# Optimization experiments

Measured on AMD Instinct MI355X. Metric: run time of the kernel, lower is better.

The kernel has to match this reference:

```python
import jax, jax.numpy as jnp
import numpy as np

EPS = 1e-12

def setup_inputs() -> dict:
    key = jax.random.key(0)
    k1, k2, k3 = jax.random.split(key, 3)
    B, D, N, NCLS = 1024, 512, 100000, 1000
    z = jax.random.normal(k1, (B, D), dtype=jnp.float32)
    lab_bank = jax.random.normal(k2, (N, D), dtype=jnp.float32)
    lab_labels = jax.random.randint(k3, (N,), 0, NCLS, dtype=jnp.int64)
    return {"z": z, "lab_bank": lab_bank, "lab_labels": lab_labels, "topk": 5}

def reference(z, lab_bank, lab_labels, topk):
    # cosine similarity: normalize query and bank, then GEMM
    zn = z / jnp.maximum(jnp.linalg.norm(z, axis=-1, keepdims=True), EPS)            # [B, D]
    bn = lab_bank / jnp.maximum(jnp.linalg.norm(lab_bank, axis=-1, keepdims=True), EPS)  # [N, D]
    sim = jnp.einsum('bd,nd->bn', zn, bn)                                            # [B, N]
    top_vals, top_idx = jax.lax.top_k(sim, topk)                                     # [B, k] each
    labels = lab_labels[top_idx]                                                     # [B, k]
    return top_idx, top_vals, labels
```

## Files before the change

kernel.cpp:

```cpp
#include <hip/hip_runtime.h>
#include <math.h>

#define DDIM 512
#define NS 96
#define SPITCH 132
#define KMASK 0xFFFFF800
#define NEG_INF (-3.0e38f)
#define IMAX 0x7fffffff

typedef __fp16   h16x2 __attribute__((ext_vector_type(2)));
typedef _Float16 f16x8 __attribute__((ext_vector_type(8)));
typedef float    f32x4 __attribute__((ext_vector_type(4)));
typedef int      i32x4 __attribute__((ext_vector_type(4)));

__device__ __forceinline__ int imin(int a, int b) { return a < b ? a : b; }
__device__ __forceinline__ int imax(int a, int b) { return a > b ? a : b; }

__device__ __forceinline__ void glds16(const void* g, void* l) {
    __builtin_amdgcn_global_load_lds((const __attribute__((address_space(1))) void*)g,
                                     (__attribute__((address_space(3))) void*)l, 16, 0, 0);
}

__global__ __launch_bounds__(256) void split_tile_k(const float* __restrict__ src,
                                                    unsigned* __restrict__ tile,
                                                    float* __restrict__ rn, int rows) {
    const int t = threadIdx.x;
    const int r = t >> 1, hf = t & 1;
    const int R = blockIdx.x * 128 + r;
    const bool valid = R < rows;
    const float* srow = src + (size_t)(valid ? R : 0) * DDIM + hf * 16;
    float ss = 0.f;
    for (int ks = 0; ks < 16; ++ks) {
        float4 v0 = *(const float4*)(srow + ks * 32);
        float4 v1 = *(const float4*)(srow + ks * 32 + 4);
        float4 v2 = *(const float4*)(srow + ks * 32 + 8);
        float4 v3 = *(const float4*)(srow + ks * 32 + 12);
        ss += v0.x*v0.x + v0.y*v0.y + v0.z*v0.z + v0.w*v0.w
            + v1.x*v1.x + v1.y*v1.y + v1.z*v1.z + v1.w*v1.w
            + v2.x*v2.x + v2.y*v2.y + v2.z*v2.z + v2.w*v2.w
            + v3.x*v3.x + v3.y*v3.y + v3.z*v3.z + v3.w*v3.w;
        unsigned o[8];
        o[0] = __builtin_bit_cast(unsigned, __builtin_amdgcn_cvt_pkrtz(v0.x, v0.y));
        o[1] = __builtin_bit_cast(unsigned, __builtin_amdgcn_cvt_pkrtz(v0.z, v0.w));
        o[2] = __builtin_bit_cast(unsigned, __builtin_amdgcn_cvt_pkrtz(v1.x, v1.y));
        o[3] = __builtin_bit_cast(unsigned, __builtin_amdgcn_cvt_pkrtz(v1.z, v1.w));
        o[4] = __builtin_bit_cast(unsigned, __builtin_amdgcn_cvt_pkrtz(v2.x, v2.y));
        o[5] = __builtin_bit_cast(unsigned, __builtin_amdgcn_cvt_pkrtz(v2.z, v2.w));
        o[6] = __builtin_bit_cast(unsigned, __builtin_amdgcn_cvt_pkrtz(v3.x, v3.y));
        o[7] = __builtin_bit_cast(unsigned, __builtin_amdgcn_cvt_pkrtz(v3.z, v3.w));
        if (!valid) {
            #pragma unroll
            for (int q = 0; q < 8; ++q) o[q] = 0u;
        }
        unsigned* dst = tile + ((size_t)(blockIdx.x * 16 + ks) * 128 + r) * 16 + hf * 8;
        *(i32x4*)dst       = *(i32x4*)o;
        *(i32x4*)(dst + 4) = *(i32x4*)(o + 4);
    }
    ss += __shfl_xor(ss, 1, 64);
    if (valid && hf == 0) rn[R] = 1.0f / fmaxf(sqrtf(ss), 1e-12f);
}

__global__ __launch_bounds__(256, 3) void gemm_screen_k(
    const unsigned* __restrict__ zh, const unsigned* __restrict__ bh,
    const float* __restrict__ rb,
    int* __restrict__ cand, int N, int nChunks) {

    __shared__ alignas(16) int smem[8448];
    int* SIMI = smem;

    const int t = threadIdx.x;
    const int w = t >> 6, lane = t & 63;
    const int wm = w & 1, wn = w >> 1;
    const int quad = lane >> 4, l16 = lane & 15;
    const int split = blockIdx.x, rowblk = blockIdx.y;
    const int soff = w * 1024 + lane * 16;

    int t0 = (int)0x80000000, t1 = t0, t2 = t0, t3 = t0;

    int iter = 0;
    for (int chunk = split; chunk < nChunks; chunk += NS, ++iter) {
        f32x4 acc[4][4];
        #pragma unroll
        for (int mi = 0; mi < 4; ++mi)
            #pragma unroll
            for (int ni = 0; ni < 4; ++ni) acc[mi][ni] = (f32x4){0.f, 0.f, 0.f, 0.f};

        for (int ks = 0; ks < 16; ++ks) {
            __syncthreads();
            const char* gA = (const char*)zh + ((size_t)(rowblk * 16 + ks) * 8192);
            const char* gB = (const char*)bh + ((size_t)(chunk * 16 + ks) * 8192);
            glds16(gA + soff,        (char*)smem + soff);
            glds16(gA + 4096 + soff, (char*)smem + 4096 + soff);
            glds16(gB + soff,        (char*)smem + 8192 + soff);
            glds16(gB + 4096 + soff, (char*)smem + 12288 + soff);
            __syncthreads();

            const unsigned short* A  = (const unsigned short*)smem;
            const unsigned short* Bb = (const unsigned short*)((char*)smem + 8192);
            f16x8 af[4], bf[4];
            #pragma unroll
            for (int mi = 0; mi < 4; ++mi)
                af[mi] = __builtin_bit_cast(f16x8,
                    *(const i32x4*)(A + (wm * 64 + mi * 16 + l16) * 32 + quad * 8));
            #pragma unroll
            for (int ni = 0; ni < 4; ++ni)
                bf[ni] = __builtin_bit_cast(f16x8,
                    *(const i32x4*)(Bb + (wn * 64 + ni * 16 + l16) * 32 + quad * 8));
            #pragma unroll
            for (int mi = 0; mi < 4; ++mi)
                #pragma unroll
                for (int ni = 0; ni < 4; ++ni)
                    acc[mi][ni] = __builtin_amdgcn_mfma_f32_16x16x32_f16(af[mi], bf[ni], acc[mi][ni], 0, 0, 0);
        }

        const int colBase = chunk * 128;
        const int iterTag = iter << 7;
        #pragma unroll
        for (int p = 0; p < 2; ++p) {
            __syncthreads();
            #pragma unroll
            for (int nj = 0; nj < 2; ++nj) {
                const int ni = p * 2 + nj;
                const int cCol = wn * 64 + ni * 16 + l16;
                const float rbv = rb[colBase + cCol];
                const int cp = wn * 32 + nj * 16 + l16;
                #pragma unroll
                for (int mi = 0; mi < 4; ++mi) {
                    i32x4 kv;
                    #pragma unroll
                    for (int rr = 0; rr < 4; ++rr) {
                        float v = acc[mi][ni][rr] * rbv;
                        kv[rr] = (__float_as_int(v) & KMASK) | cCol;
                    }
                    *(i32x4*)(SIMI + cp * SPITCH + wm * 64 + mi * 16 + quad * 4) = kv;
                }
            }
            __syncthreads();
            {
                const int r = t >> 1, h = t & 1;
                const int* s = SIMI + (h * 32) * SPITCH + r;
                #pragma unroll
                for (int j = 0; j < 32; ++j) {
                    int kk = s[j * SPITCH] | iterTag;
                    int k1 = imin(kk, t0); t0 = imax(kk, t0);
                    int k2 = imin(k1, t1); t1 = imax(k1, t1);
                    int k3 = imin(k2, t2); t2 = imax(k2, t2);
                    t3 = imax(k3, t3);
                }
            }
        }
    }

    const int r = t >> 1, h = t & 1;
    i32x4 outk = { t0, t1, t2, t3 };
    *(i32x4*)(cand + (((size_t)(rowblk * 128 + r) * NS + split) * 2 + h) * 4) = outk;
}

__global__ __launch_bounds__(256) void merge_rescore_k(
    const int* __restrict__ cand,
    const float* __restrict__ z, const float* __restrict__ bank,
    const float* __restrict__ rz, const float* __restrict__ rb,
    const int* __restrict__ labels, float* __restrict__ out, int BK, int N) {

    __shared__ float zrow[DDIM];
    __shared__ int   idxs[32];
    __shared__ float dots[32];

    const int row = blockIdx.x;
    const int t = threadIdx.x, w = t >> 6, lane = t & 63;

    {   float2 v = *(const float2*)(z + (size_t)row * DDIM + t * 2);
        zrow[t * 2] = v.x; zrow[t * 2 + 1] = v.y; }

    if (w == 0) {
        int k[12];
        const int* cp = cand + (size_t)row * (NS * 2 * 4) + lane * 12;
        #pragma unroll
        for (int q = 0; q < 12; ++q) k[q] = cp[q];
        for (int r = 0; r < 32; ++r) {
            int lk = k[0], lq = 0;
            #pragma unroll
            for (int q = 1; q < 12; ++q) if (k[q] > lk) { lk = k[q]; lq = q; }
            int wk = lk, wl = lane, wq = lq;
            #pragma unroll
            for (int off = 32; off > 0; off >>= 1) {
                int ok = __shfl_xor(wk, off, 64);
                int ol = __shfl_xor(wl, off, 64);
                int oq = __shfl_xor(wq, off, 64);
                if (ok > wk || (ok == wk && ol < wl)) { wk = ok; wl = ol; wq = oq; }
            }
            if (lane == wl) {
                #pragma unroll
                for (int q = 0; q < 12; ++q) if (q == wq) k[q] = (int)0x80000000;
            }
            if (lane == 0) {
                int j = wl * 12 + wq;
                int split = j >> 3;
                int c = wk & 127, it = (wk >> 7) & 15;
                int gi = (it * NS + split) * 128 + c;
                idxs[r] = gi < N ? gi : 0;
            }
        }
    }
    __syncthreads();

    #pragma unroll
    for (int jj = 0; jj < 8; ++jj) {
        const int ci = idxs[w * 8 + jj];
        const float* br = bank + (size_t)ci * DDIM + lane * 8;
        float4 x0 = *(const float4*)br;
        float4 x1 = *(const float4*)(br + 4);
        const float* zz = zrow + lane * 8;
        float4 z0 = *(const float4*)zz;
        float4 z1 = *(const float4*)(zz + 4);
        float s = x0.x*z0.x + x0.y*z0.y + x0.z*z0.z + x0.w*z0.w
                + x1.x*z1.x + x1.y*z1.y + x1.z*z1.z + x1.w*z1.w;
        #pragma unroll
        for (int off = 32; off > 0; off >>= 1) s += __shfl_xor(s, off, 64);
        if (lane == 0) dots[w * 8 + jj] = s;
    }
    __syncthreads();

    if (w == 0) {
        const float rzv = rz[row];
        float v; int ii;
        if (lane < 32) { ii = idxs[lane]; v = dots[lane] * rzv * rb[ii]; }
        else           { ii = IMAX;       v = NEG_INF; }
        for (int r = 0; r < 5; ++r) {
            float bv = v; int bi = ii;
            #pragma unroll
            for (int off = 32; off > 0; off >>= 1) {
                float ov = __shfl_xor(bv, off, 64);
                int   oi = __shfl_xor(bi, off, 64);
                if (ov > bv || (ov == bv && oi < bi)) { bv = ov; bi = oi; }
            }
            if (v == bv && ii == bi) { v = NEG_INF; ii = IMAX; }
            if (lane == 0) {
                out[(size_t)row * 5 + r]          = (float)bi;
                out[BK + (size_t)row * 5 + r]     = bv;
                out[2 * BK + (size_t)row * 5 + r] = (float)labels[bi];
            }
        }
    }
}

extern "C" void kernel_launch(void* const* d_in, const int* in_sizes, int n_in,
                              void* d_out, int out_size, void* d_ws, size_t ws_size,
                              hipStream_t stream) {
    const float* z    = (const float*)d_in[0];
    const float* bank = (const float*)d_in[1];
    const int*   lab  = (const int*)d_in[2];
    const int B = in_sizes[0] / DDIM;
    const int N = in_sizes[1] / DDIM;
    const int BK = out_size / 3;
    const int nChunks = (N + 127) >> 7;
    float* out = (float*)d_out;
    char* ws = (char*)d_ws;

    const size_t o_rz = 0;
    const size_t o_rb = 4096;
    const size_t o_zh = o_rb + (size_t)nChunks * 128 * 4;
    const size_t o_bh = o_zh + (size_t)(B / 128) * 16 * 8192;
    const size_t o_cv = o_bh + (size_t)nChunks * 16 * 8192;

    float* rz = (float*)(ws + o_rz);
    float* rb = (float*)(ws + o_rb);
    unsigned* zh = (unsigned*)(ws + o_zh);
    unsigned* bh = (unsigned*)(ws + o_bh);
    int* cand = (int*)(ws + o_cv);

    split_tile_k<<<nChunks, 256, 0, stream>>>(bank, bh, rb, N);
    split_tile_k<<<B / 128, 256, 0, stream>>>(z, zh, rz, B);
    gemm_screen_k<<<dim3(NS, B / 128), 256, 0, stream>>>(zh, bh, rb, cand, N, nChunks);
    merge_rescore_k<<<B, 256, 0, stream>>>(cand, z, bank, rz, rb, lab, out, BK, N);
}
```

Before: 545.4 us.

## Double-buffer GEMM LDS tiles with prefetch, custom barriers, med3 top-4 insert

Moves the per-k-step global-to-LDS loads into a double-buffered pipeline. The next k-slice, or the first slice of the next chunk, is prefetched while MFMAs run on the current buffer, and the two syncthreads per step become one barrier that waits only on vmcnt. It also hoists the rb loads to the start of the chunk, folds the iteration tag into the key before the LDS write, and replaces the top-4 insertion min/max chain with v_med3_i32. LDS use grows and the SIMI buffer is moved past the first A tile, which may cut occupancy, and the hand-written waitcnt barriers need correct ordering to stay race-free.

```diff
diff --git a/kernel.cpp b/kernel.cpp
--- a/kernel.cpp
+++ b/kernel.cpp
@@ -8,7 +8,6 @@
 #define NEG_INF (-3.0e38f)
 #define IMAX 0x7fffffff
 
-typedef __fp16   h16x2 __attribute__((ext_vector_type(2)));
 typedef _Float16 f16x8 __attribute__((ext_vector_type(8)));
 typedef float    f32x4 __attribute__((ext_vector_type(4)));
 typedef int      i32x4 __attribute__((ext_vector_type(4)));
@@ -16,10 +15,23 @@
 __device__ __forceinline__ int imin(int a, int b) { return a < b ? a : b; }
 __device__ __forceinline__ int imax(int a, int b) { return a > b ? a : b; }
 
+__device__ __forceinline__ int med3(int a, int b, int c) {
+    int d;
+    asm("v_med3_i32 %0, %1, %2, %3" : "=v"(d) : "v"(a), "v"(b), "v"(c));
+    return d;
+}
+
 __device__ __forceinline__ void glds16(const void* g, void* l) {
     __builtin_amdgcn_global_load_lds((const __attribute__((address_space(1))) void*)g,
                                      (__attribute__((address_space(3))) void*)l, 16, 0, 0);
 }
+
+#define KBAR() do { asm volatile("s_waitcnt vmcnt(0)" ::: "memory"); \
+                    __builtin_amdgcn_s_barrier();                    \
+                    asm volatile("" ::: "memory"); } while (0)
+#define EBAR() do { asm volatile("s_waitcnt lgkmcnt(0)" ::: "memory"); \
+                    __builtin_amdgcn_s_barrier();                      \
+                    asm volatile("" ::: "memory"); } while (0)
 
 __global__ __launch_bounds__(256) void split_tile_k(const float* __restrict__ src,
                                                     unsigned* __restrict__ tile,
@@ -57,7 +69,7 @@
         *(i32x4*)(dst + 4) = *(i32x4*)(o + 4);
     }
     ss += __shfl_xor(ss, 1, 64);
-    if (valid && hf == 0) rn[R] = 1.0f / fmaxf(sqrtf(ss), 1e-12f);
+    if (hf == 0) rn[R] = valid ? 1.0f / fmaxf(sqrtf(ss), 1e-12f) : 0.0f;
 }
 
 __global__ __launch_bounds__(256, 3) void gemm_screen_k(
@@ -65,8 +77,8 @@
     const float* __restrict__ rb,
     int* __restrict__ cand, int N, int nChunks) {
 
-    __shared__ alignas(16) int smem[8448];
-    int* SIMI = smem;
+    __shared__ alignas(16) int smem[12544];
+    int* SIMI = smem + 4096;
 
     const int t = threadIdx.x;
     const int w = t >> 6, lane = t & 63;
@@ -77,6 +89,15 @@
 
     int t0 = (int)0x80000000, t1 = t0, t2 = t0, t3 = t0;
 
+    {
+        const char* gA = (const char*)zh + (size_t)(rowblk * 16) * 8192;
+        const char* gB = (const char*)bh + (size_t)(split * 16) * 8192;
+        glds16(gA + soff,        (char*)smem + soff);
+        glds16(gA + 4096 + soff, (char*)smem + 4096 + soff);
+        glds16(gB + soff,        (char*)smem + 8192 + soff);
+        glds16(gB + 4096 + soff, (char*)smem + 12288 + soff);
+    }
+
     int iter = 0;
     for (int chunk = split; chunk < nChunks; chunk += NS, ++iter) {
         f32x4 acc[4][4];
@@ -84,19 +105,35 @@
         for (int mi = 0; mi < 4; ++mi)
             #pragma unroll
             for (int ni = 0; ni < 4; ++ni) acc[mi][ni] = (f32x4){0.f, 0.f, 0.f, 0.f};
-
+        float rbv[4];
+
+        #pragma unroll 2
         for (int ks = 0; ks < 16; ++ks) {
-            __syncthreads();
-            const char* gA = (const char*)zh + ((size_t)(rowblk * 16 + ks) * 8192);
-            const char* gB = (const char*)bh + ((size_t)(chunk * 16 + ks) * 8192);
-            glds16(gA + soff,        (char*)smem + soff);
-            glds16(gA + 4096 + soff, (char*)smem + 4096 + soff);
-            glds16(gB + soff,        (char*)smem + 8192 + soff);
-            glds16(gB + 4096 + soff, (char*)smem + 12288 + soff);
-            __syncthreads();
-
-            const unsigned short* A  = (const unsigned short*)smem;
-            const unsigned short* Bb = (const unsigned short*)((char*)smem + 8192);
+            KBAR();
+            if (ks < 15) {
+                const char* gA = (const char*)zh + (size_t)(rowblk * 16 + ks + 1) * 8192;
+                const char* gB = (const char*)bh + (size_t)(chunk * 16 + ks + 1) * 8192;
+                char* l = (char*)smem + (((ks & 1) ^ 1) << 14);
+                glds16(gA + soff,        l + soff);
+                glds16(gA + 4096 + soff, l + 4096 + soff);
+                glds16(gB + soff,        l + 8192 + soff);
+                glds16(gB + 4096 + soff, l + 12288 + soff);
+            } else if (chunk + NS < nChunks) {
+                const char* gA = (const char*)zh + (size_t)(rowblk * 16) * 8192;
+                const char* gB = (const char*)bh + (size_t)((chunk + NS) * 16) * 8192;
+                glds16(gA + soff,        (char*)smem + soff);
+                glds16(gA + 4096 + soff, (char*)smem + 4096 + soff);
+                glds16(gB + soff,        (char*)smem + 8192 + soff);
+                glds16(gB + 4096 + soff, (char*)smem + 12288 + soff);
+            }
+            if (ks == 0) {
+                #pragma unroll
+                for (int ni = 0; ni < 4; ++ni)
+                    rbv[ni] = rb[chunk * 128 + wn * 64 + ni * 16 + l16];
+            }
+
+            const unsigned short* A  = (const unsigned short*)((const char*)smem + ((ks & 1) << 14));
+            const unsigned short* Bb = (const unsigned short*)((const char*)smem + ((ks & 1) << 14) + 8192);
             f16x8 af[4], bf[4];
             #pragma unroll
             for (int mi = 0; mi < 4; ++mi)
@@ -113,39 +150,40 @@
                     acc[mi][ni] = __builtin_amdgcn_mfma_f32_16x16x32_f16(af[mi], bf[ni], acc[mi][ni], 0, 0, 0);
         }
 
-        const int colBase = chunk * 128;
         const int iterTag = iter << 7;
         #pragma unroll
         for (int p = 0; p < 2; ++p) {
-            __syncthreads();
+            EBAR();
             #pragma unroll
             for (int nj = 0; nj < 2; ++nj) {
                 const int ni = p * 2 + nj;
                 const int cCol = wn * 64 + ni * 16 + l16;
-                const float rbv = rb[colBase + cCol];
+                const int tagc = iterTag | cCol;
+                const float rv = rbv[ni];
                 const int cp = wn * 32 + nj * 16 + l16;
                 #pragma unroll
                 for (int mi = 0; mi < 4; ++mi) {
                     i32x4 kv;
                     #pragma unroll
                     for (int rr = 0; rr < 4; ++rr) {
-                        float v = acc[mi][ni][rr] * rbv;
-                        kv[rr] = (__float_as_int(v) & KMASK) | cCol;
+                        float v = acc[mi][ni][rr] * rv;
+                        kv[rr] = (__float_as_int(v) & KMASK) | tagc;
                     }
                     *(i32x4*)(SIMI + cp * SPITCH + wm * 64 + mi * 16 + quad * 4) = kv;
                 }
             }
-            __syncthreads();
+            EBAR();
             {
                 const int r = t >> 1, h = t & 1;
                 const int* s = SIMI + (h * 32) * SPITCH + r;
                 #pragma unroll
                 for (int j = 0; j < 32; ++j) {
-                    int kk = s[j * SPITCH] | iterTag;
-                    int k1 = imin(kk, t0); t0 = imax(kk, t0);
-                    int k2 = imin(k1, t1); t1 = imax(k1, t1);
-                    int k3 = imin(k2, t2); t2 = imax(k2, t2);
-                    t3 = imax(k3, t3);
+                    int kk = s[j * SPITCH];
+                    int n1 = med3(kk, t0, t1);
+                    int n2 = med3(kk, t1, t2);
+                    int n3 = med3(kk, t2, t3);
+                    t0 = imax(kk, t0);
+                    t1 = n1; t2 = n2; t3 = n3;
                 }
             }
         }
```

Measured after the change: 484.1 us. 11.2% less time.
